# Performance work log

Measured on AMD Instinct MI355X. Metric: run time of the kernel, lower is better.

## Reference

```python
import jax, jax.numpy as jnp
import numpy as np


def setup_inputs() -> dict:
    key = jax.random.key(0)
    B, D = 1024, 65536
    inputs = jax.random.normal(key, (B, D), dtype=jnp.float32)
    return {"inputs": inputs, "k": 1024}


def reference(inputs, k):
    # top_k along last axis (matches tf.math.top_k)
    top_k_vals, _ = jax.lax.top_k(inputs, k)          # [B, k]
    # tf.math.reduce_min with no axis -> global scalar threshold
    threshold = jnp.min(top_k_vals)
    mask = jnp.where(inputs >= threshold, jnp.float32(1.0), jnp.float32(0.0))
    return mask * inputs
```

## Files before the change

### kernel.cpp

```cpp
#include <hip/hip_runtime.h>
#include <stdint.h>

#define TPB 256
#define NBH 2048
#define NB3 1024
#define CAP 6144
#define DCOLS 65536
#define NSAMP 4096

typedef float f4 __attribute__((ext_vector_type(4)));

__device__ __forceinline__ unsigned f2key(float f) {
  unsigned u = __float_as_uint(f);
  unsigned m = ((int)u >> 31) | 0x80000000u;
  return u ^ m;
}
__device__ __forceinline__ float key2f(unsigned k) {
  unsigned u = (k & 0x80000000u) ? (k ^ 0x80000000u) : ~k;
  return __uint_as_float(u);
}

__device__ __forceinline__ void clear_hist(unsigned* hist, int NB) {
  for (int i = threadIdx.x; i < NB; i += TPB) hist[i] = 0u;
}

__device__ void find_top(const unsigned* hist, int NB, unsigned K,
                         unsigned* scan, unsigned* selbin, unsigned* selrem) {
  const int tid = threadIdx.x;
  const int C = NB / TPB;
  unsigned cs = 0;
  for (int i = 0; i < C; ++i) cs += hist[tid * C + i];
  scan[tid] = cs;
  __syncthreads();
  if (tid < 64) {
    unsigned e0 = scan[tid * 4 + 0], e1 = scan[tid * 4 + 1];
    unsigned e2 = scan[tid * 4 + 2], e3 = scan[tid * 4 + 3];
    unsigned s = e0 + e1 + e2 + e3;
    unsigned suff = s;
    for (int off = 1; off < 64; off <<= 1) {
      unsigned t = __shfl_down(suff, off);
      if (tid + off < 64) suff += t;
    }
    unsigned tail = suff - s;
    scan[tid * 4 + 3] = e3 + tail;
    scan[tid * 4 + 2] = e2 + e3 + tail;
    scan[tid * 4 + 1] = e1 + e2 + e3 + tail;
    scan[tid * 4 + 0] = s + tail;
  }
  __syncthreads();
  unsigned suff = scan[tid];
  unsigned above = suff - cs;
  if (above < K && suff >= K) {
    unsigned cAbove = above;
    for (int bin = tid * C + C - 1; bin >= tid * C; --bin) {
      unsigned c = hist[bin];
      if (cAbove + c >= K) { *selbin = (unsigned)bin; *selrem = K - cAbove; break; }
      cAbove += c;
    }
  }
  __syncthreads();
}

__global__ void __launch_bounds__(TPB, 4)
topk_select(const float* __restrict__ in, const int* __restrict__ kptr,
            unsigned* __restrict__ thr) {
  __shared__ unsigned hist[NBH];
  __shared__ unsigned scan[TPB];
  __shared__ unsigned cand[CAP];
  __shared__ unsigned sel_bin, sel_rem, cand_cnt;

  const int tid = threadIdx.x;
  const int lane = tid & 63;
  const int row = blockIdx.x;
  const unsigned K = (unsigned)(*kptr);
  const f4* rowv = (const f4*)(in + (size_t)row * DCOLS);
  const int n4 = DCOLS / 4;

  clear_hist(hist, NBH);
  if (tid == 0) cand_cnt = 0u;
  __syncthreads();
  {
    f4 s0 = rowv[tid], s1 = rowv[tid + TPB];
    f4 s2 = rowv[tid + 2 * TPB], s3 = rowv[tid + 3 * TPB];
#define HSAMP(v)                                                               \
    atomicAdd(&hist[f2key(v.x) >> 21], 1u);                                    \
    atomicAdd(&hist[f2key(v.y) >> 21], 1u);                                    \
    atomicAdd(&hist[f2key(v.z) >> 21], 1u);                                    \
    atomicAdd(&hist[f2key(v.w) >> 21], 1u);
    HSAMP(s0) HSAMP(s1) HSAMP(s2) HSAMP(s3)
#undef HSAMP
  }
  __syncthreads();
  unsigned ksamp = K >> 3;
  if (ksamp < 32u) ksamp = 32u;
  if (ksamp > NSAMP - 1) ksamp = NSAMP - 1;
  find_top(hist, NBH, ksamp, scan, &sel_bin, &sel_rem);
  const unsigned tlo = sel_bin << 21;
  __syncthreads();

#define CPCT(kk)                                                               \
    {                                                                          \
      bool p = (kk) >= tlo;                                                    \
      unsigned long long m = __ballot(p);                                      \
      if (m) {                                                                 \
        unsigned base = 0;                                                     \
        if (lane == 0) base = atomicAdd(&cand_cnt, (unsigned)__popcll(m));     \
        base = __shfl(base, 0);                                                \
        if (p) {                                                               \
          unsigned off = base + (unsigned)__popcll(m & ((1ull << lane) - 1ull));\
          if (off < CAP) cand[off] = (kk);                                     \
        }                                                                      \
      }                                                                        \
    }
#define PROC(v)                                                                \
    {                                                                          \
      unsigned kx = f2key(v.x), ky = f2key(v.y);                               \
      unsigned kz = f2key(v.z), kw = f2key(v.w);                               \
      bool any = (kx >= tlo) | (ky >= tlo) | (kz >= tlo) | (kw >= tlo);        \
      if (__ballot(any)) { CPCT(kx) CPCT(ky) CPCT(kz) CPCT(kw) }               \
    }
  for (int base = 0; base < n4; base += TPB * 4) {
    f4 v0 = rowv[base + tid];
    f4 v1 = rowv[base + tid + TPB];
    f4 v2 = rowv[base + tid + 2 * TPB];
    f4 v3 = rowv[base + tid + 3 * TPB];
    PROC(v0) PROC(v1) PROC(v2) PROC(v3)
  }
#undef PROC
  __syncthreads();
  const unsigned nc = cand_cnt;
  __syncthreads();

  unsigned rk;
  if (nc >= K && nc <= CAP) {
    clear_hist(hist, NBH); __syncthreads();
    for (unsigned i = tid; i < nc; i += TPB) atomicAdd(&hist[cand[i] >> 21], 1u);
    __syncthreads();
    find_top(hist, NBH, K, scan, &sel_bin, &sel_rem);
    const unsigned b1 = sel_bin, K2 = sel_rem;
    __syncthreads();

    clear_hist(hist, NBH); __syncthreads();
    for (unsigned i = tid; i < nc; i += TPB) {
      unsigned kk = cand[i];
      if ((kk >> 21) == b1) atomicAdd(&hist[(kk >> 10) & (NBH - 1)], 1u);
    }
    __syncthreads();
    find_top(hist, NBH, K2, scan, &sel_bin, &sel_rem);
    const unsigned b2 = sel_bin, K3 = sel_rem;
    __syncthreads();

    clear_hist(hist, NB3); __syncthreads();
    const unsigned pfx = (b1 << 11) | b2;
    for (unsigned i = tid; i < nc; i += TPB) {
      unsigned kk = cand[i];
      if ((kk >> 10) == pfx) atomicAdd(&hist[kk & (NB3 - 1)], 1u);
    }
    __syncthreads();
    find_top(hist, NB3, K3, scan, &sel_bin, &sel_rem);
    rk = (b1 << 21) | (b2 << 10) | sel_bin;
  } else {
    clear_hist(hist, NBH); __syncthreads();
    for (int i = tid; i < n4; i += TPB) {
      f4 v = rowv[i];
      atomicAdd(&hist[f2key(v.x) >> 21], 1u);
      atomicAdd(&hist[f2key(v.y) >> 21], 1u);
      atomicAdd(&hist[f2key(v.z) >> 21], 1u);
      atomicAdd(&hist[f2key(v.w) >> 21], 1u);
    }
    __syncthreads();
    find_top(hist, NBH, K, scan, &sel_bin, &sel_rem);
    const unsigned b1 = sel_bin, K2 = sel_rem;
    __syncthreads();

    clear_hist(hist, NBH); __syncthreads();
    for (int i = tid; i < n4; i += TPB) {
      f4 v = rowv[i];
      unsigned kk;
      kk = f2key(v.x); if ((kk >> 21) == b1) atomicAdd(&hist[(kk >> 10) & (NBH - 1)], 1u);
      kk = f2key(v.y); if ((kk >> 21) == b1) atomicAdd(&hist[(kk >> 10) & (NBH - 1)], 1u);
      kk = f2key(v.z); if ((kk >> 21) == b1) atomicAdd(&hist[(kk >> 10) & (NBH - 1)], 1u);
      kk = f2key(v.w); if ((kk >> 21) == b1) atomicAdd(&hist[(kk >> 10) & (NBH - 1)], 1u);
    }
    __syncthreads();
    find_top(hist, NBH, K2, scan, &sel_bin, &sel_rem);
    const unsigned b2 = sel_bin, K3 = sel_rem;
    __syncthreads();

    clear_hist(hist, NB3); __syncthreads();
    const unsigned pfx = (b1 << 11) | b2;
    for (int i = tid; i < n4; i += TPB) {
      f4 v = rowv[i];
      unsigned kk;
      kk = f2key(v.x); if ((kk >> 10) == pfx) atomicAdd(&hist[kk & (NB3 - 1)], 1u);
      kk = f2key(v.y); if ((kk >> 10) == pfx) atomicAdd(&hist[kk & (NB3 - 1)], 1u);
      kk = f2key(v.z); if ((kk >> 10) == pfx) atomicAdd(&hist[kk & (NB3 - 1)], 1u);
      kk = f2key(v.w); if ((kk >> 10) == pfx) atomicAdd(&hist[kk & (NB3 - 1)], 1u);
    }
    __syncthreads();
    find_top(hist, NB3, K3, scan, &sel_bin, &sel_rem);
    rk = (b1 << 21) | (b2 << 10) | sel_bin;
  }
#undef CPCT
  if (tid == 0) atomicMin(thr, rk);
}

__global__ void __launch_bounds__(TPB)
maskk(const f4* __restrict__ in, f4* __restrict__ out,
      const unsigned* __restrict__ thrkey, int n4) {
  const float thr = key2f(thrkey[0]);
  int idx = blockIdx.x * TPB + threadIdx.x;
  int stride = gridDim.x * TPB;
  for (int i = idx; i < n4; i += stride) {
    f4 v = in[i];
    f4 o;
    o.x = (v.x >= thr) ? v.x : 0.0f;
    o.y = (v.y >= thr) ? v.y : 0.0f;
    o.z = (v.z >= thr) ? v.z : 0.0f;
    o.w = (v.w >= thr) ? v.w : 0.0f;
    __builtin_nontemporal_store(o, &out[i]);
  }
}

extern "C" void kernel_launch(void* const* d_in, const int* in_sizes, int n_in,
                              void* d_out, int out_size, void* d_ws, size_t ws_size,
                              hipStream_t stream) {
  const float* in = (const float*)d_in[0];
  const int* kptr = (const int*)d_in[1];
  f4* out = (f4*)d_out;
  unsigned* thr = (unsigned*)d_ws;

  const int B = in_sizes[0] / DCOLS;
  const int n4 = out_size / 4;

  hipMemsetAsync(thr, 0xFF, 4, stream);
  hipLaunchKernelGGL(topk_select, dim3(B), dim3(TPB), 0, stream, in, kptr, thr);
  hipLaunchKernelGGL(maskk, dim3(4096), dim3(TPB), 0, stream,
                     (const f4*)in, out, thr, n4);
}
```

Measured before the change: 482.9 us.

## Fuse masking into the select pass with a fixed prefilter and sparse fixup

The select kernel now writes the masked output during its single streaming pass, keeping only values at or above a fixed key (float 2.0). It also records each row's candidate keys and column indices in workspace. A second per-row kernel zeroes only the candidates below the final global threshold. It falls back to a full re-mask when the threshold falls below the fixed key or a row overflowed or underfilled its candidate set. This removes the separate full read of the input for masking. The cost is candidate writes and a constant tuned to the expected value distribution, with a slow fallback if that assumption fails.

New measurement: 492.9 us. +2.1%, slower.

```diff
diff --git a/kernel.cpp b/kernel.cpp
--- a/kernel.cpp
+++ b/kernel.cpp
@@ -4,9 +4,9 @@
 #define TPB 256
 #define NBH 2048
 #define NB3 1024
-#define CAP 6144
+#define CAP 4096
 #define DCOLS 65536
-#define NSAMP 4096
+#define TLOKEY 0xC0000000u
 
 typedef float f4 __attribute__((ext_vector_type(4)));
 
@@ -62,11 +62,14 @@
 }
 
 __global__ void __launch_bounds__(TPB, 4)
-topk_select(const float* __restrict__ in, const int* __restrict__ kptr,
-            unsigned* __restrict__ thr) {
+select_prune(const float* __restrict__ in, const int* __restrict__ kptr,
+             float* __restrict__ out, unsigned* __restrict__ thr,
+             unsigned* __restrict__ ncand, unsigned* __restrict__ rowbad,
+             unsigned long long* __restrict__ gcand) {
+  __shared__ unsigned ckey[CAP];
+  __shared__ unsigned short cidx[CAP];
   __shared__ unsigned hist[NBH];
   __shared__ unsigned scan[TPB];
-  __shared__ unsigned cand[CAP];
   __shared__ unsigned sel_bin, sel_rem, cand_cnt;
 
   const int tid = threadIdx.x;
@@ -74,33 +77,15 @@
   const int row = blockIdx.x;
   const unsigned K = (unsigned)(*kptr);
   const f4* rowv = (const f4*)(in + (size_t)row * DCOLS);
+  f4* outv = (f4*)(out + (size_t)row * DCOLS);
   const int n4 = DCOLS / 4;
 
-  clear_hist(hist, NBH);
   if (tid == 0) cand_cnt = 0u;
   __syncthreads();
-  {
-    f4 s0 = rowv[tid], s1 = rowv[tid + TPB];
-    f4 s2 = rowv[tid + 2 * TPB], s3 = rowv[tid + 3 * TPB];
-#define HSAMP(v)                                                               \
-    atomicAdd(&hist[f2key(v.x) >> 21], 1u);                                    \
-    atomicAdd(&hist[f2key(v.y) >> 21], 1u);                                    \
-    atomicAdd(&hist[f2key(v.z) >> 21], 1u);                                    \
-    atomicAdd(&hist[f2key(v.w) >> 21], 1u);
-    HSAMP(s0) HSAMP(s1) HSAMP(s2) HSAMP(s3)
-#undef HSAMP
-  }
-  __syncthreads();
-  unsigned ksamp = K >> 3;
-  if (ksamp < 32u) ksamp = 32u;
-  if (ksamp > NSAMP - 1) ksamp = NSAMP - 1;
-  find_top(hist, NBH, ksamp, scan, &sel_bin, &sel_rem);
-  const unsigned tlo = sel_bin << 21;
-  __syncthreads();
-
-#define CPCT(kk)                                                               \
+
+#define CPCT(kk, ei)                                                           \
     {                                                                          \
-      bool p = (kk) >= tlo;                                                    \
+      bool p = (kk) >= TLOKEY;                                                 \
       unsigned long long m = __ballot(p);                                      \
       if (m) {                                                                 \
         unsigned base = 0;                                                     \
@@ -108,33 +93,52 @@
         base = __shfl(base, 0);                                                \
         if (p) {                                                               \
           unsigned off = base + (unsigned)__popcll(m & ((1ull << lane) - 1ull));\
-          if (off < CAP) cand[off] = (kk);                                     \
+          if (off < CAP) { ckey[off] = (kk); cidx[off] = (unsigned short)(ei); }\
         }                                                                      \
       }                                                                        \
     }
-#define PROC(v)                                                                \
+#define PROC(v, vno)                                                           \
     {                                                                          \
       unsigned kx = f2key(v.x), ky = f2key(v.y);                               \
       unsigned kz = f2key(v.z), kw = f2key(v.w);                               \
-      bool any = (kx >= tlo) | (ky >= tlo) | (kz >= tlo) | (kw >= tlo);        \
-      if (__ballot(any)) { CPCT(kx) CPCT(ky) CPCT(kz) CPCT(kw) }               \
+      f4 o;                                                                    \
+      o.x = (kx >= TLOKEY) ? v.x : 0.0f;                                       \
+      o.y = (ky >= TLOKEY) ? v.y : 0.0f;                                       \
+      o.z = (kz >= TLOKEY) ? v.z : 0.0f;                                       \
+      o.w = (kw >= TLOKEY) ? v.w : 0.0f;                                       \
+      __builtin_nontemporal_store(o, &outv[vno]);                              \
+      bool any = (kx >= TLOKEY) | (ky >= TLOKEY) | (kz >= TLOKEY) |            \
+                 (kw >= TLOKEY);                                               \
+      if (__ballot(any)) {                                                     \
+        CPCT(kx, (vno) * 4 + 0) CPCT(ky, (vno) * 4 + 1)                        \
+        CPCT(kz, (vno) * 4 + 2) CPCT(kw, (vno) * 4 + 3)                        \
+      }                                                                        \
     }
   for (int base = 0; base < n4; base += TPB * 4) {
-    f4 v0 = rowv[base + tid];
-    f4 v1 = rowv[base + tid + TPB];
-    f4 v2 = rowv[base + tid + 2 * TPB];
-    f4 v3 = rowv[base + tid + 3 * TPB];
-    PROC(v0) PROC(v1) PROC(v2) PROC(v3)
+    int i0 = base + tid;
+    f4 v0 = rowv[i0];
+    f4 v1 = rowv[i0 + TPB];
+    f4 v2 = rowv[i0 + 2 * TPB];
+    f4 v3 = rowv[i0 + 3 * TPB];
+    PROC(v0, i0) PROC(v1, i0 + TPB) PROC(v2, i0 + 2 * TPB) PROC(v3, i0 + 3 * TPB)
   }
 #undef PROC
+#undef CPCT
   __syncthreads();
   const unsigned nc = cand_cnt;
   __syncthreads();
+
+  const unsigned nstore = (nc < CAP) ? nc : CAP;
+  for (unsigned i = tid; i < nstore; i += TPB) {
+    unsigned long long e = ((unsigned long long)ckey[i] << 32) | cidx[i];
+    __builtin_nontemporal_store(e, &gcand[(size_t)row * CAP + i]);
+  }
+  if (tid == 0) ncand[row] = nstore;
 
   unsigned rk;
   if (nc >= K && nc <= CAP) {
     clear_hist(hist, NBH); __syncthreads();
-    for (unsigned i = tid; i < nc; i += TPB) atomicAdd(&hist[cand[i] >> 21], 1u);
+    for (unsigned i = tid; i < nc; i += TPB) atomicAdd(&hist[ckey[i] >> 21], 1u);
     __syncthreads();
     find_top(hist, NBH, K, scan, &sel_bin, &sel_rem);
     const unsigned b1 = sel_bin, K2 = sel_rem;
@@ -142,7 +146,7 @@
 
     clear_hist(hist, NBH); __syncthreads();
     for (unsigned i = tid; i < nc; i += TPB) {
-      unsigned kk = cand[i];
+      unsigned kk = ckey[i];
       if ((kk >> 21) == b1) atomicAdd(&hist[(kk >> 10) & (NBH - 1)], 1u);
     }
     __syncthreads();
@@ -153,13 +157,14 @@
     clear_hist(hist, NB3); __syncthreads();
     const unsigned pfx = (b1 << 11) | b2;
     for (unsigned i = tid; i < nc; i += TPB) {
-      unsigned kk = cand[i];
+      unsigned kk = ckey[i];
       if ((kk >> 10) == pfx) atomicAdd(&hist[kk & (NB3 - 1)], 1u);
     }
     __syncthreads();
     find_top(hist, NB3, K3, scan, &sel_bin, &sel_rem);
     rk = (b1 << 21) | (b2 << 10) | sel_bin;
   } else {
+    if (tid == 0) rowbad[row] = 1u;
     clear_hist(hist, NBH); __syncthreads();
     for (int i = tid; i < n4; i += TPB) {
       f4 v = rowv[i];
@@ -201,24 +206,38 @@
     find_top(hist, NB3, K3, scan, &sel_bin, &sel_rem);
     rk = (b1 << 21) | (b2 << 10) | sel_bin;
   }
-#undef CPCT
   if (tid == 0) atomicMin(thr, rk);
 }
 
 __global__ void __launch_bounds__(TPB)
-maskk(const f4* __restrict__ in, f4* __restrict__ out,
-      const unsigned* __restrict__ thrkey, int n4) {
-  const float thr = key2f(thrkey[0]);
-  int idx = blockIdx.x * TPB + threadIdx.x;
-  int stride = gridDim.x * TPB;
-  for (int i = idx; i < n4; i += stride) {
-    f4 v = in[i];
-    f4 o;
-    o.x = (v.x >= thr) ? v.x : 0.0f;
-    o.y = (v.y >= thr) ? v.y : 0.0f;
-    o.z = (v.z >= thr) ? v.z : 0.0f;
-    o.w = (v.w >= thr) ? v.w : 0.0f;
-    __builtin_nontemporal_store(o, &out[i]);
+prune_tail(const float* __restrict__ in, float* __restrict__ out,
+           const unsigned* __restrict__ thr, const unsigned* __restrict__ ncand,
+           const unsigned* __restrict__ rowbad,
+           const unsigned long long* __restrict__ gcand) {
+  const int tid = threadIdx.x;
+  const int row = blockIdx.x;
+  const unsigned thrk = thr[0];
+
+  if (thrk >= TLOKEY && !rowbad[row]) {
+    const unsigned n = ncand[row];
+    for (unsigned i = tid; i < n; i += TPB) {
+      unsigned long long e = gcand[(size_t)row * CAP + i];
+      if ((unsigned)(e >> 32) < thrk)
+        out[(size_t)row * DCOLS + (unsigned)(e & 0xFFFFu)] = 0.0f;
+    }
+  } else {
+    const float thrf = key2f(thrk);
+    const f4* rowv = (const f4*)(in + (size_t)row * DCOLS);
+    f4* outv = (f4*)(out + (size_t)row * DCOLS);
+    for (int i = tid; i < DCOLS / 4; i += TPB) {
+      f4 v = rowv[i];
+      f4 o;
+      o.x = (v.x >= thrf) ? v.x : 0.0f;
+      o.y = (v.y >= thrf) ? v.y : 0.0f;
+      o.z = (v.z >= thrf) ? v.z : 0.0f;
+      o.w = (v.w >= thrf) ? v.w : 0.0f;
+      outv[i] = o;
+    }
   }
 }
 
@@ -227,14 +246,19 @@
                               hipStream_t stream) {
   const float* in = (const float*)d_in[0];
   const int* kptr = (const int*)d_in[1];
-  f4* out = (f4*)d_out;
+  float* out = (float*)d_out;
+
   unsigned* thr = (unsigned*)d_ws;
+  unsigned* ncand = (unsigned*)d_ws + 64;
+  unsigned* rowbad = (unsigned*)d_ws + 64 + 1024;
+  unsigned long long* gcand = (unsigned long long*)((char*)d_ws + 16384);
 
   const int B = in_sizes[0] / DCOLS;
-  const int n4 = out_size / 4;
 
   hipMemsetAsync(thr, 0xFF, 4, stream);
-  hipLaunchKernelGGL(topk_select, dim3(B), dim3(TPB), 0, stream, in, kptr, thr);
-  hipLaunchKernelGGL(maskk, dim3(4096), dim3(TPB), 0, stream,
-                     (const f4*)in, out, thr, n4);
-}
+  hipMemsetAsync((char*)d_ws + 256, 0, 8192, stream);
+  hipLaunchKernelGGL(select_prune, dim3(B), dim3(TPB), 0, stream,
+                     in, kptr, out, thr, ncand, rowbad, gcand);
+  hipLaunchKernelGGL(prune_tail, dim3(B), dim3(TPB), 0, stream,
+                     in, out, thr, ncand, rowbad, gcand);
+}
```
